# Optimization experiments

Hardware: AMD Instinct MI355X
Metric: run time of the kernel (lower is better)

## Reference

```python
import jax, jax.numpy as jnp
import numpy as np

B = 64
IN_F = 8192
OUT_F = 8192
DEG = 7          # Chebyshev degree -> DEG+1 basis functions
NNZ = 262144     # number of edges in the sparse connectivity (avg fan-in 32)
EPS = 1e-7


def setup_inputs() -> dict:
    key = jax.random.key(0)
    k1, k2, k3, k4 = jax.random.split(key, 4)
    x = jax.random.normal(k1, (B, IN_F), dtype=jnp.float32)
    edge_rows = jax.random.randint(k2, (NNZ,), 0, OUT_F, dtype=jnp.int32)
    edge_cols = jax.random.randint(k3, (NNZ,), 0, IN_F, dtype=jnp.int32)
    # learned sparse-linear values: one weight per edge per Chebyshev order
    weight = jax.random.normal(k4, (NNZ, DEG + 1), dtype=jnp.float32) * 0.02
    return {"x": x, "weight": weight, "edge_rows": edge_rows, "edge_cols": edge_cols}


def reference(x, weight, edge_rows, edge_cols):
    # Chebyshev basis via trigonometric identity: T_k(t) = cos(k * acos(t))
    t = jnp.clip(jnp.tanh(x), -1.0 + EPS, 1.0 - EPS)            # [B, IN_F]
    theta = jnp.arccos(t)                                        # [B, IN_F]
    ks = jnp.arange(DEG + 1, dtype=x.dtype)                      # [D+1]
    cheb = jnp.cos(theta[:, :, None] * ks)                       # [B, IN_F, D+1]
    # sparse linear over the degree-expanded features:
    # y[b, r] = sum_{e: rows[e]==r} sum_d weight[e, d] * cheb[b, cols[e], d]
    basis = cheb[:, edge_cols, :]                                # [B, NNZ, D+1] (irregular gather)
    contrib = jnp.einsum('bnd,nd->bn', basis, weight)            # [B, NNZ]
    y = jax.ops.segment_sum(contrib.T, edge_rows, num_segments=OUT_F).T  # [B, OUT_F]
    return y
```

## Files before the change

kernel.cpp:

```cpp
#include <hip/hip_runtime.h>

#define IN_F 8192
#define OUT_F 8192
#define NNZ 262144
#define EPS 1e-7f
#define SLOTS 80

#define WS_TT   0
#define WS_CNT  (2u << 20)
#define WS_SCOL ((2u << 20) + (64u << 10))
#define WS_SW   (8u << 20)

__global__ __launch_bounds__(256) void prep_kernel(
    const float* __restrict__ x, const float* __restrict__ w,
    const int* __restrict__ rows, const int* __restrict__ cols,
    float* __restrict__ tT, int* __restrict__ cnt,
    int* __restrict__ sCol, float4* __restrict__ sW) {
  const int tid = threadIdx.x;
  if (blockIdx.x < 128) {
    __shared__ float lds[64 * 65];
    const int f0 = blockIdx.x * 64;
#pragma unroll
    for (int i = 0; i < 16; ++i) {
      int idx = tid + i * 256;
      int f = idx & 63;
      int b = idx >> 6;
      float v = tanhf(x[b * IN_F + f0 + f]);
      v = fminf(fmaxf(v, -1.0f + EPS), 1.0f - EPS);
      lds[f * 65 + b] = v;
    }
    __syncthreads();
#pragma unroll
    for (int i = 0; i < 16; ++i) {
      int idx = tid + i * 256;
      int b = idx & 63;
      int f = idx >> 6;
      tT[(f0 + f) * 64 + b] = lds[f * 65 + b];
    }
  } else {
    const int e = (blockIdx.x - 128) * 256 + tid;
    const int r = rows[e];
    const int c = cols[e];
    const float4* w4 = (const float4*)w;
    const float4 wa = w4[2 * e];
    const float4 wb = w4[2 * e + 1];
    const int p = atomicAdd(&cnt[r], 1);
    if (p < SLOTS) {
      const int s = r * SLOTS + p;
      sCol[s] = c;
      sW[2 * s] = wa;
      sW[2 * s + 1] = wb;
    }
  }
}

__device__ __forceinline__ float cheb_dot(const float* __restrict__ tT,
                                          const float4* __restrict__ sW,
                                          int slot, int ci, int lane) {
  const float4 wa = sW[2 * slot];
  const float4 wb = sW[2 * slot + 1];
  const float t = tT[((unsigned)ci << 6) + lane];
  const float t2 = t + t;
  float Tm = t;
  float Tc = fmaf(t2, t, -1.0f);
  float acc = fmaf(wa.y, t, wa.x);
  acc = fmaf(wa.z, Tc, acc);
  float Tn = fmaf(t2, Tc, -Tm);
  acc = fmaf(wa.w, Tn, acc);
  Tm = Tc; Tc = Tn;
  Tn = fmaf(t2, Tc, -Tm);
  acc = fmaf(wb.x, Tn, acc);
  Tm = Tc; Tc = Tn;
  Tn = fmaf(t2, Tc, -Tm);
  acc = fmaf(wb.y, Tn, acc);
  Tm = Tc; Tc = Tn;
  Tn = fmaf(t2, Tc, -Tm);
  acc = fmaf(wb.z, Tn, acc);
  Tm = Tc; Tc = Tn;
  Tn = fmaf(t2, Tc, -Tm);
  acc = fmaf(wb.w, Tn, acc);
  return acc;
}

__global__ __launch_bounds__(256) void gather_kernel(
    const float* __restrict__ tT, const int* __restrict__ cnt,
    const int* __restrict__ sCol, const float4* __restrict__ sW,
    float* __restrict__ y) {
  __shared__ float tile[4 * 65];
  const int tid = threadIdx.x;
  const int lane = tid & 63;
  const int wv = tid >> 6;
  const int r0 = blockIdx.x * 4;
  const int row = __builtin_amdgcn_readfirstlane(r0 + wv);
  const int n = min(__builtin_amdgcn_readfirstlane(cnt[row]), SLOTS);
  const int base = row * SLOTS;
  float acc = 0.0f;
  for (int s = 0; s < n; s += 64) {
    int cv = 0;
    if (s + lane < n) cv = sCol[base + s + lane];
    const int m = min(64, n - s);
    int i = 0;
    for (; i + 4 <= m; i += 4) {
      const int c0 = __builtin_amdgcn_readlane(cv, i);
      const int c1 = __builtin_amdgcn_readlane(cv, i + 1);
      const int c2 = __builtin_amdgcn_readlane(cv, i + 2);
      const int c3 = __builtin_amdgcn_readlane(cv, i + 3);
      const int sl = base + s + i;
      const float a0 = cheb_dot(tT, sW, sl + 0, c0, lane);
      const float a1 = cheb_dot(tT, sW, sl + 1, c1, lane);
      const float a2 = cheb_dot(tT, sW, sl + 2, c2, lane);
      const float a3 = cheb_dot(tT, sW, sl + 3, c3, lane);
      acc += (a0 + a1) + (a2 + a3);
    }
    for (; i < m; ++i) {
      const int c0 = __builtin_amdgcn_readlane(cv, i);
      acc += cheb_dot(tT, sW, base + s + i, c0, lane);
    }
  }
  tile[wv * 65 + lane] = acc;
  __syncthreads();
  const int rr = tid & 3;
  const int b = tid >> 2;
  y[b * OUT_F + r0 + rr] = tile[rr * 65 + b];
}

extern "C" void kernel_launch(void* const* d_in, const int* in_sizes, int n_in,
                              void* d_out, int out_size, void* d_ws, size_t ws_size,
                              hipStream_t stream) {
  const float* x    = (const float*)d_in[0];
  const float* w    = (const float*)d_in[1];
  const int*   rows = (const int*)d_in[2];
  const int*   cols = (const int*)d_in[3];
  float* y = (float*)d_out;

  char* ws = (char*)d_ws;
  float*  tT   = (float*)(ws + WS_TT);
  int*    cnt  = (int*)(ws + WS_CNT);
  int*    sCol = (int*)(ws + WS_SCOL);
  float4* sW   = (float4*)(ws + WS_SW);

  hipMemsetAsync(cnt, 0, OUT_F * sizeof(int), stream);
  prep_kernel<<<128 + NNZ / 256, 256, 0, stream>>>(x, w, rows, cols, tT, cnt, sCol, sW);
  gather_kernel<<<OUT_F / 4, 256, 0, stream>>>(tT, cnt, sCol, sW, y);
}
```

Measured before the change: 102.8 us.

## Fuse memset, prep and gather into one cooperative kernel with grid syncs

```diff
diff --git a/kernel.cpp b/kernel.cpp
--- a/kernel.cpp
+++ b/kernel.cpp
@@ -1,58 +1,19 @@
 #include <hip/hip_runtime.h>
+#include <hip/hip_cooperative_groups.h>
+
+namespace cg = cooperative_groups;
 
 #define IN_F 8192
 #define OUT_F 8192
 #define NNZ 262144
 #define EPS 1e-7f
 #define SLOTS 80
+#define NBLK 1024
 
 #define WS_TT   0
 #define WS_CNT  (2u << 20)
 #define WS_SCOL ((2u << 20) + (64u << 10))
 #define WS_SW   (8u << 20)
-
-__global__ __launch_bounds__(256) void prep_kernel(
-    const float* __restrict__ x, const float* __restrict__ w,
-    const int* __restrict__ rows, const int* __restrict__ cols,
-    float* __restrict__ tT, int* __restrict__ cnt,
-    int* __restrict__ sCol, float4* __restrict__ sW) {
-  const int tid = threadIdx.x;
-  if (blockIdx.x < 128) {
-    __shared__ float lds[64 * 65];
-    const int f0 = blockIdx.x * 64;
-#pragma unroll
-    for (int i = 0; i < 16; ++i) {
-      int idx = tid + i * 256;
-      int f = idx & 63;
-      int b = idx >> 6;
-      float v = tanhf(x[b * IN_F + f0 + f]);
-      v = fminf(fmaxf(v, -1.0f + EPS), 1.0f - EPS);
-      lds[f * 65 + b] = v;
-    }
-    __syncthreads();
-#pragma unroll
-    for (int i = 0; i < 16; ++i) {
-      int idx = tid + i * 256;
-      int b = idx & 63;
-      int f = idx >> 6;
-      tT[(f0 + f) * 64 + b] = lds[f * 65 + b];
-    }
-  } else {
-    const int e = (blockIdx.x - 128) * 256 + tid;
-    const int r = rows[e];
-    const int c = cols[e];
-    const float4* w4 = (const float4*)w;
-    const float4 wa = w4[2 * e];
-    const float4 wb = w4[2 * e + 1];
-    const int p = atomicAdd(&cnt[r], 1);
-    if (p < SLOTS) {
-      const int s = r * SLOTS + p;
-      sCol[s] = c;
-      sW[2 * s] = wa;
-      sW[2 * s + 1] = wb;
-    }
-  }
-}
 
 __device__ __forceinline__ float cheb_dot(const float* __restrict__ tT,
                                           const float4* __restrict__ sW,
@@ -82,46 +43,99 @@
   return acc;
 }
 
-__global__ __launch_bounds__(256) void gather_kernel(
-    const float* __restrict__ tT, const int* __restrict__ cnt,
-    const int* __restrict__ sCol, const float4* __restrict__ sW,
+__global__ __launch_bounds__(256, 4) void fused_kernel(
+    const float* __restrict__ x, const float* __restrict__ w,
+    const int* __restrict__ rows, const int* __restrict__ cols,
+    float* __restrict__ tT, int* __restrict__ cnt,
+    int* __restrict__ sCol, float4* __restrict__ sW,
     float* __restrict__ y) {
-  __shared__ float tile[4 * 65];
+  cg::grid_group grid = cg::this_grid();
+  __shared__ float lds[64 * 65];
   const int tid = threadIdx.x;
+  const int bid = blockIdx.x;
+
+  if (tid < 8) cnt[bid * 8 + tid] = 0;
+  grid.sync();
+
+  if (bid < 128) {
+    const int f0 = bid * 64;
+#pragma unroll
+    for (int i = 0; i < 16; ++i) {
+      int idx = tid + i * 256;
+      int f = idx & 63;
+      int b = idx >> 6;
+      float v = tanhf(x[b * IN_F + f0 + f]);
+      v = fminf(fmaxf(v, -1.0f + EPS), 1.0f - EPS);
+      lds[f * 65 + b] = v;
+    }
+    __syncthreads();
+#pragma unroll
+    for (int i = 0; i < 16; ++i) {
+      int idx = tid + i * 256;
+      int b = idx & 63;
+      int f = idx >> 6;
+      tT[(f0 + f) * 64 + b] = lds[f * 65 + b];
+    }
+  }
+
+  {
+    const int e = bid * 256 + tid;
+    const int r = rows[e];
+    const int c = cols[e];
+    const float4* w4 = (const float4*)w;
+    const float4 wa = w4[2 * e];
+    const float4 wb = w4[2 * e + 1];
+    const int p = atomicAdd(&cnt[r], 1);
+    if (p < SLOTS) {
+      const int s = r * SLOTS + p;
+      sCol[s] = c;
+      sW[2 * s] = wa;
+      sW[2 * s + 1] = wb;
+    }
+  }
+  grid.sync();
+
   const int lane = tid & 63;
   const int wv = tid >> 6;
-  const int r0 = blockIdx.x * 4;
-  const int row = __builtin_amdgcn_readfirstlane(r0 + wv);
-  const int n = min(__builtin_amdgcn_readfirstlane(cnt[row]), SLOTS);
-  const int base = row * SLOTS;
-  float acc = 0.0f;
-  for (int s = 0; s < n; s += 64) {
-    int cv = 0;
-    if (s + lane < n) cv = sCol[base + s + lane];
-    const int m = min(64, n - s);
-    int i = 0;
-    for (; i + 4 <= m; i += 4) {
-      const int c0 = __builtin_amdgcn_readlane(cv, i);
-      const int c1 = __builtin_amdgcn_readlane(cv, i + 1);
-      const int c2 = __builtin_amdgcn_readlane(cv, i + 2);
-      const int c3 = __builtin_amdgcn_readlane(cv, i + 3);
-      const int sl = base + s + i;
-      const float a0 = cheb_dot(tT, sW, sl + 0, c0, lane);
-      const float a1 = cheb_dot(tT, sW, sl + 1, c1, lane);
-      const float a2 = cheb_dot(tT, sW, sl + 2, c2, lane);
-      const float a3 = cheb_dot(tT, sW, sl + 3, c3, lane);
-      acc += (a0 + a1) + (a2 + a3);
+  const int r0 = bid * 8;
+  for (int half = 0; half < 2; ++half) {
+    const int rr = wv + half * 4;
+    const int row = __builtin_amdgcn_readfirstlane(r0 + rr);
+    const int n = min(__builtin_amdgcn_readfirstlane(cnt[row]), SLOTS);
+    const int base = row * SLOTS;
+    float acc = 0.0f;
+    for (int s = 0; s < n; s += 64) {
+      int cv = 0;
+      if (s + lane < n) cv = sCol[base + s + lane];
+      const int m = min(64, n - s);
+      int i = 0;
+      for (; i + 4 <= m; i += 4) {
+        const int c0 = __builtin_amdgcn_readlane(cv, i);
+        const int c1 = __builtin_amdgcn_readlane(cv, i + 1);
+        const int c2 = __builtin_amdgcn_readlane(cv, i + 2);
+        const int c3 = __builtin_amdgcn_readlane(cv, i + 3);
+        const int sl = base + s + i;
+        const float a0 = cheb_dot(tT, sW, sl + 0, c0, lane);
+        const float a1 = cheb_dot(tT, sW, sl + 1, c1, lane);
+        const float a2 = cheb_dot(tT, sW, sl + 2, c2, lane);
+        const float a3 = cheb_dot(tT, sW, sl + 3, c3, lane);
+        acc += (a0 + a1) + (a2 + a3);
+      }
+      for (; i < m; ++i) {
+        const int c0 = __builtin_amdgcn_readlane(cv, i);
+        acc += cheb_dot(tT, sW, base + s + i, c0, lane);
+      }
     }
-    for (; i < m; ++i) {
-      const int c0 = __builtin_amdgcn_readlane(cv, i);
-      acc += cheb_dot(tT, sW, base + s + i, c0, lane);
-    }
+    lds[rr * 65 + lane] = acc;
   }
-  tile[wv * 65 + lane] = acc;
   __syncthreads();
-  const int rr = tid & 3;
-  const int b = tid >> 2;
-  y[b * OUT_F + r0 + rr] = tile[rr * 65 + b];
+#pragma unroll
+  for (int it = 0; it < 2; ++it) {
+    const int idx = tid + it * 256;
+    const int rr = idx & 7;
+    const int b = idx >> 3;
+    y[b * OUT_F + r0 + rr] = lds[rr * 65 + b];
+  }
 }
 
 extern "C" void kernel_launch(void* const* d_in, const int* in_sizes, int n_in,
@@ -139,7 +153,8 @@
   int*    sCol = (int*)(ws + WS_SCOL);
   float4* sW   = (float4*)(ws + WS_SW);
 
-  hipMemsetAsync(cnt, 0, OUT_F * sizeof(int), stream);
-  prep_kernel<<<128 + NNZ / 256, 256, 0, stream>>>(x, w, rows, cols, tT, cnt, sCol, sW);
-  gather_kernel<<<OUT_F / 4, 256, 0, stream>>>(tT, cnt, sCol, sW, y);
+  void* args[] = {(void*)&x, (void*)&w, (void*)&rows, (void*)&cols,
+                  (void*)&tT, (void*)&cnt, (void*)&sCol, (void*)&sW, (void*)&y};
+  hipLaunchCooperativeKernel((const void*)fused_kernel, dim3(NBLK), dim3(256),
+                             args, 0, stream);
 }
```

New measurement: 305.1 us. +196.8%, slower.
